# Kernel optimization log

Hardware: AMD Instinct MI355X
Metric: run time of the kernel (lower is better)

The kernel has to match this reference:

```python
import jax, jax.numpy as jnp
import numpy as np
from math import sqrt

E = 1024          # embedding_size
A = 64            # attention_size (per-head)
H = E // A        # 16 heads
FF = 4 * E        # 4096
B, S = 2, 2048
EPS = 1e-5


def layernorm(x, g, b):
    mu = jnp.mean(x, axis=-1, keepdims=True)
    var = jnp.mean(jnp.square(x - mu), axis=-1, keepdims=True)
    return (x - mu) * jax.lax.rsqrt(var + EPS) * g + b


def setup_inputs() -> dict:
    key = jax.random.key(0)
    ks = jax.random.split(key, 12)
    s = 0.02
    return {
        "embedding": jax.random.normal(ks[0], (B, S, E), jnp.float32),
        "positional_encoding": jax.random.normal(ks[1], (B, S, E), jnp.float32),
        # per-head QKV projections (no bias), stacked over heads: [H, E, A]
        "Wq": jax.random.normal(ks[2], (H, E, A), jnp.float32) * s,
        "Wk": jax.random.normal(ks[3], (H, E, A), jnp.float32) * s,
        "Wv": jax.random.normal(ks[4], (H, E, A), jnp.float32) * s,
        "Wproj": jax.random.normal(ks[5], (E, E), jnp.float32) * s,  # no bias
        "W1": jax.random.normal(ks[6], (E, FF), jnp.float32) * s,
        "b1": jnp.zeros((FF,), jnp.float32),
        "W2": jax.random.normal(ks[7], (FF, E), jnp.float32) * s,
        "b2": jnp.zeros((E,), jnp.float32),
        # LayerNorm params: attn norm, FFN-internal norm, final FF norm
        "g_attn": jnp.ones((E,), jnp.float32), "be_attn": jnp.zeros((E,), jnp.float32),
        "g_ffn": jnp.ones((E,), jnp.float32), "be_ffn": jnp.zeros((E,), jnp.float32),
        "g_out": jnp.ones((E,), jnp.float32), "be_out": jnp.zeros((E,), jnp.float32),
    }


def reference(embedding, positional_encoding, Wq, Wk, Wv, Wproj, W1, b1, W2, b2,
              g_attn, be_attn, g_ffn, be_ffn, g_out, be_out):
    x = embedding + positional_encoding                       # [B,S,E]
    # All heads at once (original loops over heads; same math):
    Q = jnp.einsum('bse,hea->hbsa', x, Wq)                    # [H,B,S,A]
    K = jnp.einsum('bse,hea->hbsa', x, Wk)
    V = jnp.einsum('bse,hea->hbsa', x, Wv)
    # NOTE: original scales by sqrt(input dim) = sqrt(E), not sqrt(A)
    scale = sqrt(E)
    scores = jnp.einsum('hbsa,hbta->hbst', Q, K) / scale      # [H,B,S,S]
    causal = jnp.tril(jnp.ones((S, S), bool))                 # j >= k allowed
    scores = jnp.where(causal, scores, -jnp.inf)
    probs = jax.nn.softmax(scores, axis=-1)
    attn = jnp.einsum('hbst,hbta->hbsa', probs, V)            # [H,B,S,A]
    # concat heads along feature dim -> [B,S,H*A] = [B,S,E]
    attn = jnp.transpose(attn, (1, 2, 0, 3)).reshape(x.shape[0], x.shape[1], E)
    attn = attn @ Wproj                                       # linear proj, no bias
    mha = layernorm(x + attn, g_attn, be_attn)
    # FeedForward: relu applied AFTER the second linear (as in source)
    hidden = mha @ W1 + b1
    ff = jax.nn.relu(hidden @ W2 + b2)
    ff_out = layernorm(mha + ff, g_ffn, be_ffn)
    encoded = layernorm(mha + ff_out, g_out, be_out)
    return encoded, K, V
```

## Files before the change

### kernel.cpp

```cpp
#include <hip/hip_runtime.h>


typedef unsigned short u16;
typedef unsigned int u32;
typedef __bf16 bf16x8 __attribute__((ext_vector_type(8)));
typedef float f32x4 __attribute__((ext_vector_type(4)));

#define AS1 __attribute__((address_space(1)))
#define AS3 __attribute__((address_space(3)))

__device__ __forceinline__ u16 f2bf(float f) {
    return __builtin_bit_cast(u16, static_cast<__bf16>(f));
}

__device__ __forceinline__ int swz(int row) { return ((row ^ (row >> 2)) & 7) << 4; }

__device__ __forceinline__ void gload16(void* lds, const void* g) {
    __builtin_amdgcn_global_load_lds((const AS1 void*)(unsigned long long)g,
                                     (AS3 void*)(u32)(unsigned long long)lds, 16, 0, 0);
}

template <int BM, int AMODE, int OMODE>
__launch_bounds__(256, (BM == 128) ? 2 : 3)
__global__ void k_mm(const void* Ap, const u16* __restrict__ Bt, int K, int KZ,
                     float* C, float* Cp, const float* __restrict__ bias,
                     const float* resid, const float* resid2,
                     u16* oQb, float* oKf, u16* oKb, float* oVf, int relu) {
    constexpr int MF = BM / 32;
    __shared__ __align__(16) u16 As[2][BM * 64];
    __shared__ __align__(16) u16 Bs[2][128 * 64];
    const int tid = threadIdx.x;
    const int wave = tid >> 6, lane = tid & 63, quad = lane >> 4, l16 = lane & 15;
    const int wm = wave & 1, wn = wave >> 1;
    const int m0 = blockIdx.x * BM, n0 = blockIdx.y * 128;
    const int kbeg = blockIdx.z * KZ;
    const int nk = KZ / 64;

    f32x4 acc[MF][4];
#pragma unroll
    for (int mf = 0; mf < MF; ++mf)
#pragma unroll
        for (int nf = 0; nf < 4; ++nf) acc[mf][nf] = (f32x4){0.f, 0.f, 0.f, 0.f};

    auto stageA = [&](int b, int kk) {
        if constexpr (AMODE == 1) {
            const float* Af = (const float*)Ap;
#pragma unroll
            for (int i = 0; i < BM / 16; ++i) {
                const int slot = tid + i * 256;
                const int row = slot >> 4, c4 = (slot & 15) * 4;
                float4 v = *(const float4*)(Af + (long long)(m0 + row) * K + kk + c4);
                ushort4 s;
                s.x = f2bf(v.x); s.y = f2bf(v.y); s.z = f2bf(v.z); s.w = f2bf(v.w);
                *(ushort4*)((char*)As[b] + row * 128 + ((c4 * 2) ^ swz(row))) = s;
            }
        } else {
            const u16* Ab = (const u16*)Ap;
#pragma unroll
            for (int i = 0; i < BM / 32; ++i) {
                const int chunk = wave * (BM / 32) + i;
                const int row = chunk * 8 + (lane >> 3);
                const int cb = (lane & 7) * 16;
                const int e = kk + ((cb ^ swz(row)) >> 1);
                const u16* src;
                if constexpr (AMODE == 2)
                    src = Ab + (long long)(e >> 6) * 262144 + (long long)(m0 + row) * 64 + (e & 63);
                else
                    src = Ab + (long long)(m0 + row) * K + e;
                gload16((char*)As[b] + chunk * 1024, src);
            }
        }
    };
    auto stageB = [&](int b, int kk) {
#pragma unroll
        for (int i = 0; i < 4; ++i) {
            const int chunk = wave * 4 + i;
            const int row = chunk * 8 + (lane >> 3);
            const int cb = (lane & 7) * 16;
            gload16((char*)Bs[b] + chunk * 1024,
                    Bt + (long long)(n0 + row) * K + kk + ((cb ^ swz(row)) >> 1));
        }
    };

    stageA(0, kbeg);
    stageB(0, kbeg);
    int cur = 0;
    for (int t = 0; t < nk; ++t) {
        __syncthreads();
        if (t + 1 < nk) {
            stageA(cur ^ 1, kbeg + (t + 1) * 64);
            stageB(cur ^ 1, kbeg + (t + 1) * 64);
        }
#pragma unroll
        for (int ks = 0; ks < 2; ++ks) {
            bf16x8 af[MF], bfr[4];
#pragma unroll
            for (int mf = 0; mf < MF; ++mf) {
                const int row = wm * (BM / 2) + mf * 16 + l16;
                af[mf] = *(const bf16x8*)((const char*)As[cur] + row * 128 +
                                          ((ks * 64 + quad * 16) ^ swz(row)));
            }
#pragma unroll
            for (int nf = 0; nf < 4; ++nf) {
                const int row = wn * 64 + nf * 16 + l16;
                bfr[nf] = *(const bf16x8*)((const char*)Bs[cur] + row * 128 +
                                           ((ks * 64 + quad * 16) ^ swz(row)));
            }
#pragma unroll
            for (int mf = 0; mf < MF; ++mf)
#pragma unroll
                for (int nf = 0; nf < 4; ++nf)
                    acc[mf][nf] = __builtin_amdgcn_mfma_f32_16x16x32_bf16(af[mf], bfr[nf],
                                                                          acc[mf][nf], 0, 0, 0);
        }
        cur ^= 1;
    }

#pragma unroll
    for (int mf = 0; mf < MF; ++mf) {
#pragma unroll
        for (int nf = 0; nf < 4; ++nf) {
#pragma unroll
            for (int r = 0; r < 4; ++r) {
                const long long row = m0 + wm * (BM / 2) + mf * 16 + quad * 4 + r;
                const int col = n0 + wn * 64 + nf * 16 + l16;
                float v = acc[mf][nf][r];
                if constexpr (OMODE == 0) {
                    if (bias) v += bias[col];
                    if (relu) v = fmaxf(v, 0.f);
                    if (resid) v += resid[row * 1024 + col];
                    if (resid2) v += resid2[row * 1024 + col];
                    C[row * 1024 + col] = v;
                } else if constexpr (OMODE == 1) {
                    const int sel = col >> 10, h = (col >> 6) & 15, a = col & 63;
                    const long long idx = (long long)h * 262144 + row * 64 + a;
                    if (sel == 0) oQb[idx] = f2bf(v);
                    else if (sel == 1) { oKf[idx] = v; oKb[idx] = f2bf(v); }
                    else oVf[idx] = v;
                } else {
                    Cp[(long long)blockIdx.z * 1048576 + (long long)col * 1024 + row] = v;
                }
            }
        }
    }
}

__global__ void k_prep(const float* __restrict__ emb, const float* __restrict__ pos,
                       const float* __restrict__ W1, const float* __restrict__ W2,
                       const float* __restrict__ Wq, const float* __restrict__ Wk,
                       const float* __restrict__ Wv, const float* __restrict__ Wp,
                       const float* __restrict__ b2,
                       u16* __restrict__ xb, u16* __restrict__ W1b,
                       u16* __restrict__ W2t, u16* __restrict__ WBt,
                       u16* __restrict__ WpT, float* __restrict__ b12) {
    __shared__ float T[64][65];
    const int bx = blockIdx.x, tid = threadIdx.x;
    if (bx < 8192) {
        const long long i = ((long long)(bx & 4095) * 256 + tid) * 4;
        const float* a = (bx < 4096) ? emb : W1;
        u16* o = (bx < 4096) ? xb : W1b;
        float4 v = *(const float4*)(a + i);
        if (bx < 4096) {
            float4 u = *(const float4*)(pos + i);
            v.x += u.x; v.y += u.y; v.z += u.z; v.w += u.w;
        }
        ushort4 s;
        s.x = f2bf(v.x); s.y = f2bf(v.y); s.z = f2bf(v.z); s.w = f2bf(v.w);
        *(ushort4*)(o + i) = s;
        return;
    }
    if (bx == 10240) {
        float4 v = *(const float4*)(b2 + tid * 4);
        *(float4*)(b12 + tid * 4) = v;
        return;
    }
    const float* ip;
    u16* op;
    long long ldin, ldout;
    if (bx < 9216) {
        const int t = bx - 8192, x = t & 63, z = t >> 6;
        ip = W2 + (long long)z * 64 + (long long)x * 65536;
        ldin = 1024;
        op = W2t + (long long)z * 262144 + x * 64;
        ldout = 4096;
    } else {
        const int t = bx - 9216, x = t & 15, z = t >> 4;
        const int w = z >> 4, h = z & 15;
        if (w < 3) {
            ip = (w == 0 ? Wq : (w == 1 ? Wk : Wv)) + h * 65536 + x * 4096;
            ldin = 64;
            op = WBt + (long long)(w * 16 + h) * 65536 + x * 64;
        } else {
            ip = Wp + x * 65536 + h * 64;
            ldin = 1024;
            op = WpT + (long long)h * 65536 + x * 64;
        }
        ldout = 1024;
    }
#pragma unroll
    for (int i = 0; i < 4; ++i) {
        const int slot = tid + i * 256;
        const int r = slot >> 4, c4 = (slot & 15) * 4;
        float4 v = *(const float4*)(ip + (long long)r * ldin + c4);
        T[r][c4] = v.x; T[r][c4 + 1] = v.y; T[r][c4 + 2] = v.z; T[r][c4 + 3] = v.w;
    }
    __syncthreads();
#pragma unroll
    for (int i = 0; i < 4; ++i) {
        const int slot = tid + i * 256;
        const int c = slot >> 4, r4 = (slot & 15) * 4;
        ushort4 s;
        s.x = f2bf(T[r4][c]); s.y = f2bf(T[r4 + 1][c]);
        s.z = f2bf(T[r4 + 2][c]); s.w = f2bf(T[r4 + 3][c]);
        *(ushort4*)(op + (long long)c * ldout + r4) = s;
    }
}

__global__ void k_tc(const float* __restrict__ in, u16* __restrict__ out,
                     long long ldin, long long ldout, long long szin, long long szout) {
    __shared__ float T[64][65];
    const int x = blockIdx.x, z = blockIdx.y, tid = threadIdx.x;
    const float* ip = in + (long long)z * szin + (long long)x * 64 * ldin;
    u16* op = out + (long long)z * szout + (long long)x * 64;
#pragma unroll
    for (int i = 0; i < 4; ++i) {
        const int slot = tid + i * 256;
        const int r = slot >> 4, c4 = (slot & 15) * 4;
        float4 v = *(const float4*)(ip + (long long)r * ldin + c4);
        T[r][c4] = v.x; T[r][c4 + 1] = v.y; T[r][c4 + 2] = v.z; T[r][c4 + 3] = v.w;
    }
    __syncthreads();
#pragma unroll
    for (int i = 0; i < 4; ++i) {
        const int slot = tid + i * 256;
        const int c = slot >> 4, r4 = (slot & 15) * 4;
        ushort4 s;
        s.x = f2bf(T[r4][c]); s.y = f2bf(T[r4 + 1][c]);
        s.z = f2bf(T[r4 + 2][c]); s.w = f2bf(T[r4 + 3][c]);
        *(ushort4*)(op + (long long)c * ldout + r4) = s;
    }
}

__global__ void k_rb(const float* __restrict__ P, u16* __restrict__ out,
                     const float* __restrict__ b1, const float* __restrict__ W2,
                     float* __restrict__ b12) {
    const int bx = blockIdx.x, tid = threadIdx.x;
    if (bx < 1024) {
        const long long i = ((long long)bx * 256 + tid) * 4;
        float4 a = *(const float4*)(P + i);
        float4 b = *(const float4*)(P + i + 1048576);
        float4 c = *(const float4*)(P + i + 2097152);
        float4 d = *(const float4*)(P + i + 3145728);
        ushort4 s;
        s.x = f2bf(a.x + b.x + c.x + d.x); s.y = f2bf(a.y + b.y + c.y + d.y);
        s.z = f2bf(a.z + b.z + c.z + d.z); s.w = f2bf(a.w + b.w + c.w + d.w);
        *(ushort4*)(out + i) = s;
    } else {
        const int z = bx - 1024;
        const int o4 = tid * 4;
        const float* Wr = W2 + (long long)z * 16384 + o4;
        float ax = 0.f, ay = 0.f, az = 0.f, aw = 0.f;
#pragma unroll
        for (int ff = 0; ff < 16; ++ff) {
            const float bb = b1[z * 16 + ff];
            float4 w = *(const float4*)(Wr + ff * 1024);
            ax += bb * w.x; ay += bb * w.y; az += bb * w.z; aw += bb * w.w;
        }
        atomicAdd(b12 + o4, ax);
        atomicAdd(b12 + o4 + 1, ay);
        atomicAdd(b12 + o4 + 2, az);
        atomicAdd(b12 + o4 + 3, aw);
    }
}

__launch_bounds__(512, 2)
__global__ void k_flash(u16* Qb, const u16* __restrict__ Kb, const u16* __restrict__ Vg) {
    __shared__ __align__(16) u16 Ks[2][64 * 64];
    __shared__ __align__(16) u16 Vs[2][64 * 64];
    __shared__ __align__(16) u16 Pb[8][16 * 64];
    const int tid = threadIdx.x;
    const int wave = tid >> 6, lane = tid & 63, quad = lane >> 4, l16 = lane & 15;
    const int hb = blockIdx.y, h = hb >> 1, b = hb & 1;
    const int xr = 15 - (int)blockIdx.x;
    const int q0 = xr * 128;
    const long long qbase = (long long)h * 262144 + (long long)b * 131072;
    u16* Qp = Qb + qbase + (long long)q0 * 64;
    const u16* Kp = Kb + qbase;
    const u16* Vp = Vg + (long long)hb * 131072;
    const float NEG = -1.0e30f;

    const int qrow = wave * 16 + l16;
    const bf16x8 aq0 = *(const bf16x8*)(Qp + qrow * 64 + quad * 8);
    const bf16x8 aq1 = *(const bf16x8*)(Qp + qrow * 64 + 32 + quad * 8);

    f32x4 o[4];
#pragma unroll
    for (int g = 0; g < 4; ++g) o[g] = (f32x4){0.f, 0.f, 0.f, 0.f};
    float mrun = NEG, lrun = 0.f;
    u16* Pw = Pb[wave];

    auto stage = [&](int bi, int k0) {
        const int row = tid >> 3;
        const int cb = (tid & 7) * 16;
        const int eo = (cb ^ swz(row)) >> 1;
        gload16((char*)Ks[bi] + tid * 16, Kp + (long long)(k0 + row) * 64 + eo);
        gload16((char*)Vs[bi] + tid * 16, Vp + (long long)row * 2048 + k0 + eo);
    };

    const int nit = 2 * xr + 2;
    stage(0, 0);
    int cur = 0;
    for (int it = 0; it < nit; ++it) {
        __syncthreads();
        if (it + 1 < nit) stage(cur ^ 1, (it + 1) * 64);
        f32x4 sc[4];
        __builtin_amdgcn_s_setprio(1);
#pragma unroll
        for (int kg = 0; kg < 4; ++kg) {
            const int krow = kg * 16 + l16;
            const bf16x8 bka = *(const bf16x8*)((const char*)Ks[cur] + krow * 128 +
                                                ((quad * 16) ^ swz(krow)));
            const bf16x8 bkb = *(const bf16x8*)((const char*)Ks[cur] + krow * 128 +
                                                ((64 + quad * 16) ^ swz(krow)));
            sc[kg] = (f32x4){0.f, 0.f, 0.f, 0.f};
            sc[kg] = __builtin_amdgcn_mfma_f32_16x16x32_bf16(bka, aq0, sc[kg], 0, 0, 0);
            sc[kg] = __builtin_amdgcn_mfma_f32_16x16x32_bf16(bkb, aq1, sc[kg], 0, 0, 0);
        }
        __builtin_amdgcn_s_setprio(0);
        const int k0 = it * 64;
        const int q = q0 + wave * 16 + l16;
        const bool edge = (it >= nit - 2);
        float vv[4][4];
        float tmax = NEG;
#pragma unroll
        for (int kg = 0; kg < 4; ++kg)
#pragma unroll
            for (int r = 0; r < 4; ++r) {
                float x = sc[kg][r] * 0.03125f;
                if (edge && (k0 + kg * 16 + quad * 4 + r > q)) x = NEG;
                vv[kg][r] = x;
                tmax = fmaxf(tmax, x);
            }
        tmax = fmaxf(tmax, __shfl_xor(tmax, 16));
        tmax = fmaxf(tmax, __shfl_xor(tmax, 32));
        if (__all(tmax - mrun <= 8.f)) {
            float rs = 0.f;
#pragma unroll
            for (int kg = 0; kg < 4; ++kg)
#pragma unroll
                for (int r = 0; r < 4; ++r) {
                    const float e = __expf(vv[kg][r] - mrun);
                    vv[kg][r] = e;
                    rs += e;
                }
            rs += __shfl_xor(rs, 16);
            rs += __shfl_xor(rs, 32);
            lrun += rs;
        } else {
            const float mn = fmaxf(mrun, tmax);
            const float alpha = __expf(mrun - mn);
            mrun = mn;
            float rs = 0.f;
#pragma unroll
            for (int kg = 0; kg < 4; ++kg)
#pragma unroll
                for (int r = 0; r < 4; ++r) {
                    const float e = __expf(vv[kg][r] - mn);
                    vv[kg][r] = e;
                    rs += e;
                }
            rs += __shfl_xor(rs, 16);
            rs += __shfl_xor(rs, 32);
            lrun = lrun * alpha + rs;
#pragma unroll
            for (int r = 0; r < 4; ++r) {
                const float ar = __shfl(alpha, quad * 4 + r, 16);
#pragma unroll
                for (int g = 0; g < 4; ++g) o[g][r] *= ar;
            }
        }
#pragma unroll
        for (int kg = 0; kg < 4; ++kg) {
            ushort4 s;
            s.x = f2bf(vv[kg][0]); s.y = f2bf(vv[kg][1]);
            s.z = f2bf(vv[kg][2]); s.w = f2bf(vv[kg][3]);
            *(ushort4*)((char*)Pw + l16 * 128 + ((kg * 32 + quad * 8) ^ swz(l16))) = s;
        }
        const bf16x8 ap0 = *(const bf16x8*)((const char*)Pw + l16 * 128 +
                                            ((quad * 16) ^ swz(l16)));
        const bf16x8 ap1 = *(const bf16x8*)((const char*)Pw + l16 * 128 +
                                            ((64 + quad * 16) ^ swz(l16)));
        __builtin_amdgcn_s_setprio(1);
#pragma unroll
        for (int g = 0; g < 4; ++g) {
            const int ar = g * 16 + l16;
            const bf16x8 bv0 = *(const bf16x8*)((const char*)Vs[cur] + ar * 128 +
                                                ((quad * 16) ^ swz(ar)));
            const bf16x8 bv1 = *(const bf16x8*)((const char*)Vs[cur] + ar * 128 +
                                                ((64 + quad * 16) ^ swz(ar)));
            o[g] = __builtin_amdgcn_mfma_f32_16x16x32_bf16(ap0, bv0, o[g], 0, 0, 0);
            o[g] = __builtin_amdgcn_mfma_f32_16x16x32_bf16(ap1, bv1, o[g], 0, 0, 0);
        }
        __builtin_amdgcn_s_setprio(0);
        cur ^= 1;
    }

#pragma unroll
    for (int r = 0; r < 4; ++r) {
        const float lr = __shfl(lrun, quad * 4 + r, 16);
        const float inv = 1.0f / lr;
        const int srow = wave * 16 + quad * 4 + r;
#pragma unroll
        for (int g = 0; g < 4; ++g)
            Qp[srow * 64 + g * 16 + l16] = f2bf(o[g][r] * inv);
    }
}

__global__ void k_ln(const float* in1, const float* in2,
                     const float* __restrict__ g, const float* __restrict__ be,
                     float* out) {
    __shared__ float red[8];
    const int m = blockIdx.x, tid = threadIdx.x, e0 = tid * 4;
    const long long bp = (long long)m * 1024;
    float4 v = *(const float4*)(in1 + bp + e0);
    if (in2) {
        float4 u = *(const float4*)(in2 + bp + e0);
        v.x += u.x; v.y += u.y; v.z += u.z; v.w += u.w;
    }
    float s1 = v.x + v.y + v.z + v.w;
    float s2 = v.x * v.x + v.y * v.y + v.z * v.z + v.w * v.w;
#pragma unroll
    for (int off = 1; off < 64; off <<= 1) { s1 += __shfl_xor(s1, off); s2 += __shfl_xor(s2, off); }
    if ((tid & 63) == 0) { red[tid >> 6] = s1; red[4 + (tid >> 6)] = s2; }
    __syncthreads();
    const float S1 = red[0] + red[1] + red[2] + red[3];
    const float S2 = red[4] + red[5] + red[6] + red[7];
    const float mean = S1 * (1.0f / 1024.0f);
    const float var = S2 * (1.0f / 1024.0f) - mean * mean;
    const float rstd = rsqrtf(var + 1e-5f);
    float4 ug = *(const float4*)(g + e0);
    float4 ub = *(const float4*)(be + e0);
    float4 o;
    o.x = (v.x - mean) * rstd * ug.x + ub.x;
    o.y = (v.y - mean) * rstd * ug.y + ub.y;
    o.z = (v.z - mean) * rstd * ug.z + ub.z;
    o.w = (v.w - mean) * rstd * ug.w + ub.w;
    *(float4*)(out + bp + e0) = o;
}

__global__ void k_ln23(const float* r2, const float* __restrict__ mha,
                       const float* __restrict__ g1, const float* __restrict__ be1,
                       const float* __restrict__ g2, const float* __restrict__ be2,
                       float* out) {
    __shared__ float red[8];
    const int m = blockIdx.x, tid = threadIdx.x, e0 = tid * 4;
    const long long bp = (long long)m * 1024;
    float4 v = *(const float4*)(r2 + bp + e0);
    float s1 = v.x + v.y + v.z + v.w;
    float s2 = v.x * v.x + v.y * v.y + v.z * v.z + v.w * v.w;
#pragma unroll
    for (int off = 1; off < 64; off <<= 1) { s1 += __shfl_xor(s1, off); s2 += __shfl_xor(s2, off); }
    if ((tid & 63) == 0) { red[tid >> 6] = s1; red[4 + (tid >> 6)] = s2; }
    __syncthreads();
    float S1 = red[0] + red[1] + red[2] + red[3];
    float S2 = red[4] + red[5] + red[6] + red[7];
    float mean = S1 * (1.0f / 1024.0f);
    float rstd = rsqrtf(S2 * (1.0f / 1024.0f) - mean * mean + 1e-5f);
    float4 ug = *(const float4*)(g1 + e0);
    float4 ub = *(const float4*)(be1 + e0);
    float4 vm = *(const float4*)(mha + bp + e0);
    float4 t;
    t.x = vm.x + (v.x - mean) * rstd * ug.x + ub.x;
    t.y = vm.y + (v.y - mean) * rstd * ug.y + ub.y;
    t.z = vm.z + (v.z - mean) * rstd * ug.z + ub.z;
    t.w = vm.w + (v.w - mean) * rstd * ug.w + ub.w;
    s1 = t.x + t.y + t.z + t.w;
    s2 = t.x * t.x + t.y * t.y + t.z * t.z + t.w * t.w;
#pragma unroll
    for (int off = 1; off < 64; off <<= 1) { s1 += __shfl_xor(s1, off); s2 += __shfl_xor(s2, off); }
    __syncthreads();
    if ((tid & 63) == 0) { red[tid >> 6] = s1; red[4 + (tid >> 6)] = s2; }
    __syncthreads();
    S1 = red[0] + red[1] + red[2] + red[3];
    S2 = red[4] + red[5] + red[6] + red[7];
    mean = S1 * (1.0f / 1024.0f);
    rstd = rsqrtf(S2 * (1.0f / 1024.0f) - mean * mean + 1e-5f);
    ug = *(const float4*)(g2 + e0);
    ub = *(const float4*)(be2 + e0);
    float4 oo;
    oo.x = (t.x - mean) * rstd * ug.x + ub.x;
    oo.y = (t.y - mean) * rstd * ug.y + ub.y;
    oo.z = (t.z - mean) * rstd * ug.z + ub.z;
    oo.w = (t.w - mean) * rstd * ug.w + ub.w;
    *(float4*)(out + bp + e0) = oo;
}

extern "C" void kernel_launch(void* const* d_in, const int* in_sizes, int n_in,
                              void* d_out, int out_size, void* d_ws, size_t ws_size,
                              hipStream_t stream) {
    (void)in_sizes; (void)n_in; (void)out_size; (void)ws_size;
    const float* emb    = (const float*)d_in[0];
    const float* pos    = (const float*)d_in[1];
    const float* Wq     = (const float*)d_in[2];
    const float* Wk     = (const float*)d_in[3];
    const float* Wv     = (const float*)d_in[4];
    const float* Wproj  = (const float*)d_in[5];
    const float* W1     = (const float*)d_in[6];
    const float* b1     = (const float*)d_in[7];
    const float* W2     = (const float*)d_in[8];
    const float* b2     = (const float*)d_in[9];
    const float* g_attn = (const float*)d_in[10];
    const float* be_attn= (const float*)d_in[11];
    const float* g_ffn  = (const float*)d_in[12];
    const float* be_ffn = (const float*)d_in[13];
    const float* g_out  = (const float*)d_in[14];
    const float* be_out = (const float*)d_in[15];

    float* enc   = (float*)d_out;
    float* out_K = enc + 4194304;
    float* out_V = enc + 8388608;
    u16* QbU  = (u16*)enc;
    u16* KbU  = (u16*)enc + 4194304;
    u16* W1b  = (u16*)enc;
    u16* W2t  = (u16*)enc + 4194304;
    float* Ppart = out_K;

    u16* wsu    = (u16*)d_ws;
    u16* WBt    = wsu;
    u16* xb     = wsu + 4194304;
    u16* VbT    = wsu;
    u16* WpT    = wsu + 8388608;
    u16* W12T   = wsu + 9437184;
    float* b12  = (float*)(wsu + 10485760);
    float* res1 = (float*)d_ws;

    k_prep<<<10241, 256, 0, stream>>>(emb, pos, W1, W2, Wq, Wk, Wv, Wproj, b2,
                                      xb, W1b, W2t, WBt, WpT, b12);
    k_mm<64, 0, 2><<<dim3(16, 8, 4), 256, 0, stream>>>(W1b, W2t, 4096, 1024,
        nullptr, Ppart, nullptr, nullptr, nullptr, nullptr, nullptr, nullptr, nullptr, 0);
    k_rb<<<1280, 256, 0, stream>>>(Ppart, W12T, b1, W2, b12);

    k_mm<128, 0, 1><<<dim3(32, 24), 256, 0, stream>>>(xb, WBt, 1024, 1024,
        nullptr, nullptr, nullptr, nullptr, nullptr, QbU, out_K, KbU, out_V, 0);
    k_tc<<<dim3(32, 32), 256, 0, stream>>>(out_V, VbT, 64, 2048, 131072, 131072);

    k_flash<<<dim3(16, 32), 512, 0, stream>>>(QbU, KbU, VbT);

    k_mm<64, 2, 0><<<dim3(64, 8), 256, 0, stream>>>(QbU, WpT, 1024, 1024,
        res1, nullptr, nullptr, emb, pos, nullptr, nullptr, nullptr, nullptr, 0);
    k_ln<<<4096, 256, 0, stream>>>(res1, nullptr, g_attn, be_attn, res1);

    k_mm<64, 1, 0><<<dim3(64, 8), 256, 0, stream>>>(res1, W12T, 1024, 1024,
        enc, nullptr, b12, res1, nullptr, nullptr, nullptr, nullptr, nullptr, 1);
    k_ln23<<<4096, 256, 0, stream>>>(enc, res1, g_ffn, be_ffn, g_out, be_out, enc);
}
```

Baseline: 364.7 us.

## Triple-buffer GEMM loads, fold softmax scale into Q, use exp2

For all GEMMs except the fp32-input one, the double-buffered k-loop becomes a three-stage LDS pipeline. It waits with an explicit vmcnt and a raw barrier, so two tiles of global-to-LDS loads stay in flight while the current tile is computed. The QKV projection moves to 64-row tiles, doubling its block count. The attention softmax scale and log2(e) are folded into Q when it is written as bf16, so the flash loop drops its per-element multiply and uses hardware exp2. The causal-mask branch is split out of the unmasked fast path. The costs are more LDS per block (which may lower occupancy), a hand-counted vmcnt that only holds for BM=64, and slightly different rounding of Q.

Result: slower. 374.8 us (+2.8%).

```diff
diff --git a/kernel.cpp b/kernel.cpp
--- a/kernel.cpp
+++ b/kernel.cpp
@@ -13,6 +13,8 @@
     return __builtin_bit_cast(u16, static_cast<__bf16>(f));
 }
 
+__device__ __forceinline__ float exp2hw(float x) { return __builtin_amdgcn_exp2f(x); }
+
 __device__ __forceinline__ int swz(int row) { return ((row ^ (row >> 2)) & 7) << 4; }
 
 __device__ __forceinline__ void gload16(void* lds, const void* g) {
@@ -20,15 +22,18 @@
                                      (AS3 void*)(u32)(unsigned long long)lds, 16, 0, 0);
 }
 
+#define QSCALE 0.0450842200886f
+
 template <int BM, int AMODE, int OMODE>
-__launch_bounds__(256, (BM == 128) ? 2 : 3)
+__launch_bounds__(256, (AMODE == 1) ? 3 : 2)
 __global__ void k_mm(const void* Ap, const u16* __restrict__ Bt, int K, int KZ,
                      float* C, float* Cp, const float* __restrict__ bias,
                      const float* resid, const float* resid2,
                      u16* oQb, float* oKf, u16* oKb, float* oVf, int relu) {
     constexpr int MF = BM / 32;
-    __shared__ __align__(16) u16 As[2][BM * 64];
-    __shared__ __align__(16) u16 Bs[2][128 * 64];
+    constexpr int NBUF = (AMODE == 1) ? 2 : 3;
+    __shared__ __align__(16) u16 As[NBUF][BM * 64];
+    __shared__ __align__(16) u16 Bs[NBUF][128 * 64];
     const int tid = threadIdx.x;
     const int wave = tid >> 6, lane = tid & 63, quad = lane >> 4, l16 = lane & 15;
     const int wm = wave & 1, wn = wave >> 1;
@@ -81,29 +86,20 @@
                     Bt + (long long)(n0 + row) * K + kk + ((cb ^ swz(row)) >> 1));
         }
     };
-
-    stageA(0, kbeg);
-    stageB(0, kbeg);
-    int cur = 0;
-    for (int t = 0; t < nk; ++t) {
-        __syncthreads();
-        if (t + 1 < nk) {
-            stageA(cur ^ 1, kbeg + (t + 1) * 64);
-            stageB(cur ^ 1, kbeg + (t + 1) * 64);
-        }
+    auto compute = [&](int b) {
 #pragma unroll
         for (int ks = 0; ks < 2; ++ks) {
             bf16x8 af[MF], bfr[4];
 #pragma unroll
             for (int mf = 0; mf < MF; ++mf) {
                 const int row = wm * (BM / 2) + mf * 16 + l16;
-                af[mf] = *(const bf16x8*)((const char*)As[cur] + row * 128 +
+                af[mf] = *(const bf16x8*)((const char*)As[b] + row * 128 +
                                           ((ks * 64 + quad * 16) ^ swz(row)));
             }
 #pragma unroll
             for (int nf = 0; nf < 4; ++nf) {
                 const int row = wn * 64 + nf * 16 + l16;
-                bfr[nf] = *(const bf16x8*)((const char*)Bs[cur] + row * 128 +
+                bfr[nf] = *(const bf16x8*)((const char*)Bs[b] + row * 128 +
                                            ((ks * 64 + quad * 16) ^ swz(row)));
             }
 #pragma unroll
@@ -113,7 +109,43 @@
                     acc[mf][nf] = __builtin_amdgcn_mfma_f32_16x16x32_bf16(af[mf], bfr[nf],
                                                                           acc[mf][nf], 0, 0, 0);
         }
-        cur ^= 1;
+    };
+
+    if constexpr (AMODE == 1) {
+        stageA(0, kbeg);
+        stageB(0, kbeg);
+        int cur = 0;
+        for (int t = 0; t < nk; ++t) {
+            __syncthreads();
+            if (t + 1 < nk) {
+                stageA(cur ^ 1, kbeg + (t + 1) * 64);
+                stageB(cur ^ 1, kbeg + (t + 1) * 64);
+            }
+            compute(cur);
+            cur ^= 1;
+        }
+    } else {
+        stageA(0, kbeg);
+        stageB(0, kbeg);
+        if (nk > 1) { stageA(1, kbeg + 64); stageB(1, kbeg + 64); }
+        int cur = 0;
+        for (int t = 0; t < nk; ++t) {
+            if (t < nk - 1) {
+                asm volatile("s_waitcnt vmcnt(6)" ::: "memory");
+            } else {
+                asm volatile("s_waitcnt vmcnt(0)" ::: "memory");
+            }
+            __builtin_amdgcn_s_barrier();
+            __builtin_amdgcn_sched_barrier(0);
+            if (t + 2 < nk) {
+                const int nxt = (cur >= 1) ? cur - 1 : cur + 2;
+                stageA(nxt, kbeg + (t + 2) * 64);
+                stageB(nxt, kbeg + (t + 2) * 64);
+            }
+            __builtin_amdgcn_sched_barrier(0);
+            compute(cur);
+            cur = (cur == 2) ? 0 : cur + 1;
+        }
     }
 
 #pragma unroll
@@ -134,7 +166,7 @@
                 } else if constexpr (OMODE == 1) {
                     const int sel = col >> 10, h = (col >> 6) & 15, a = col & 63;
                     const long long idx = (long long)h * 262144 + row * 64 + a;
-                    if (sel == 0) oQb[idx] = f2bf(v);
+                    if (sel == 0) oQb[idx] = f2bf(v * QSCALE);
                     else if (sel == 1) { oKf[idx] = v; oKb[idx] = f2bf(v); }
                     else oVf[idx] = v;
                 } else {
@@ -329,18 +361,27 @@
         __builtin_amdgcn_s_setprio(0);
         const int k0 = it * 64;
         const int q = q0 + wave * 16 + l16;
-        const bool edge = (it >= nit - 2);
         float vv[4][4];
         float tmax = NEG;
-#pragma unroll
-        for (int kg = 0; kg < 4; ++kg)
-#pragma unroll
-            for (int r = 0; r < 4; ++r) {
-                float x = sc[kg][r] * 0.03125f;
-                if (edge && (k0 + kg * 16 + quad * 4 + r > q)) x = NEG;
-                vv[kg][r] = x;
-                tmax = fmaxf(tmax, x);
-            }
+        if (it >= nit - 2) {
+#pragma unroll
+            for (int kg = 0; kg < 4; ++kg)
+#pragma unroll
+                for (int r = 0; r < 4; ++r) {
+                    float x = sc[kg][r];
+                    if (k0 + kg * 16 + quad * 4 + r > q) x = NEG;
+                    vv[kg][r] = x;
+                    tmax = fmaxf(tmax, x);
+                }
+        } else {
+#pragma unroll
+            for (int kg = 0; kg < 4; ++kg)
+#pragma unroll
+                for (int r = 0; r < 4; ++r) {
+                    vv[kg][r] = sc[kg][r];
+                    tmax = fmaxf(tmax, sc[kg][r]);
+                }
+        }
         tmax = fmaxf(tmax, __shfl_xor(tmax, 16));
         tmax = fmaxf(tmax, __shfl_xor(tmax, 32));
         if (__all(tmax - mrun <= 8.f)) {
@@ -349,7 +390,7 @@
             for (int kg = 0; kg < 4; ++kg)
 #pragma unroll
                 for (int r = 0; r < 4; ++r) {
-                    const float e = __expf(vv[kg][r] - mrun);
+                    const float e = exp2hw(vv[kg][r] - mrun);
                     vv[kg][r] = e;
                     rs += e;
                 }
@@ -358,14 +399,14 @@
             lrun += rs;
         } else {
             const float mn = fmaxf(mrun, tmax);
-            const float alpha = __expf(mrun - mn);
+            const float alpha = exp2hw(mrun - mn);
             mrun = mn;
             float rs = 0.f;
 #pragma unroll
             for (int kg = 0; kg < 4; ++kg)
 #pragma unroll
                 for (int r = 0; r < 4; ++r) {
-                    const float e = __expf(vv[kg][r] - mn);
+                    const float e = exp2hw(vv[kg][r] - mn);
                     vv[kg][r] = e;
                     rs += e;
                 }
@@ -540,7 +581,7 @@
         nullptr, Ppart, nullptr, nullptr, nullptr, nullptr, nullptr, nullptr, nullptr, 0);
     k_rb<<<1280, 256, 0, stream>>>(Ppart, W12T, b1, W2, b12);
 
-    k_mm<128, 0, 1><<<dim3(32, 24), 256, 0, stream>>>(xb, WBt, 1024, 1024,
+    k_mm<64, 0, 1><<<dim3(64, 24), 256, 0, stream>>>(xb, WBt, 1024, 1024,
         nullptr, nullptr, nullptr, nullptr, nullptr, QbU, out_K, KbU, out_V, 0);
     k_tc<<<dim3(32, 32), 256, 0, stream>>>(out_V, VbT, 64, 2048, 131072, 131072);
 
```

## Pair causal flash query tiles per block and fold softmax scale into Q

Applied to the files above, without the earlier changes.

The flash attention grid is halved, and each block now processes two query tiles (15-x and x). This gives every block the same total causal work and cuts the tail imbalance. The 1/32 softmax scale times log2(e) is folded into Q when it is stored in the QKV GEMM epilogue, so the inner loop can use a raw hardware exp2 with no per-element multiply. The mask branch is also split so non-edge iterations skip the mask test. Risks are fewer blocks in flight (256) and slight precision changes from scaling Q before the bf16 rounding.

New measurement: 356.6 us. 2.2% less time.

```diff
diff --git a/kernel.cpp b/kernel.cpp
--- a/kernel.cpp
+++ b/kernel.cpp
@@ -13,12 +13,16 @@
     return __builtin_bit_cast(u16, static_cast<__bf16>(f));
 }
 
+__device__ __forceinline__ float exp2hw(float x) { return __builtin_amdgcn_exp2f(x); }
+
 __device__ __forceinline__ int swz(int row) { return ((row ^ (row >> 2)) & 7) << 4; }
 
 __device__ __forceinline__ void gload16(void* lds, const void* g) {
     __builtin_amdgcn_global_load_lds((const AS1 void*)(unsigned long long)g,
                                      (AS3 void*)(u32)(unsigned long long)lds, 16, 0, 0);
 }
+
+#define QSCALE 0.0450842200886f
 
 template <int BM, int AMODE, int OMODE>
 __launch_bounds__(256, (BM == 128) ? 2 : 3)
@@ -81,6 +85,30 @@
                     Bt + (long long)(n0 + row) * K + kk + ((cb ^ swz(row)) >> 1));
         }
     };
+    auto compute = [&](int b) {
+#pragma unroll
+        for (int ks = 0; ks < 2; ++ks) {
+            bf16x8 af[MF], bfr[4];
+#pragma unroll
+            for (int mf = 0; mf < MF; ++mf) {
+                const int row = wm * (BM / 2) + mf * 16 + l16;
+                af[mf] = *(const bf16x8*)((const char*)As[b] + row * 128 +
+                                          ((ks * 64 + quad * 16) ^ swz(row)));
+            }
+#pragma unroll
+            for (int nf = 0; nf < 4; ++nf) {
+                const int row = wn * 64 + nf * 16 + l16;
+                bfr[nf] = *(const bf16x8*)((const char*)Bs[b] + row * 128 +
+                                           ((ks * 64 + quad * 16) ^ swz(row)));
+            }
+#pragma unroll
+            for (int mf = 0; mf < MF; ++mf)
+#pragma unroll
+                for (int nf = 0; nf < 4; ++nf)
+                    acc[mf][nf] = __builtin_amdgcn_mfma_f32_16x16x32_bf16(af[mf], bfr[nf],
+                                                                          acc[mf][nf], 0, 0, 0);
+        }
+    };
 
     stageA(0, kbeg);
     stageB(0, kbeg);
@@ -91,28 +119,7 @@
             stageA(cur ^ 1, kbeg + (t + 1) * 64);
             stageB(cur ^ 1, kbeg + (t + 1) * 64);
         }
-#pragma unroll
-        for (int ks = 0; ks < 2; ++ks) {
-            bf16x8 af[MF], bfr[4];
-#pragma unroll
-            for (int mf = 0; mf < MF; ++mf) {
-                const int row = wm * (BM / 2) + mf * 16 + l16;
-                af[mf] = *(const bf16x8*)((const char*)As[cur] + row * 128 +
-                                          ((ks * 64 + quad * 16) ^ swz(row)));
-            }
-#pragma unroll
-            for (int nf = 0; nf < 4; ++nf) {
-                const int row = wn * 64 + nf * 16 + l16;
-                bfr[nf] = *(const bf16x8*)((const char*)Bs[cur] + row * 128 +
-                                           ((ks * 64 + quad * 16) ^ swz(row)));
-            }
-#pragma unroll
-            for (int mf = 0; mf < MF; ++mf)
-#pragma unroll
-                for (int nf = 0; nf < 4; ++nf)
-                    acc[mf][nf] = __builtin_amdgcn_mfma_f32_16x16x32_bf16(af[mf], bfr[nf],
-                                                                          acc[mf][nf], 0, 0, 0);
-        }
+        compute(cur);
         cur ^= 1;
     }
 
@@ -134,7 +141,7 @@
                 } else if constexpr (OMODE == 1) {
                     const int sel = col >> 10, h = (col >> 6) & 15, a = col & 63;
                     const long long idx = (long long)h * 262144 + row * 64 + a;
-                    if (sel == 0) oQb[idx] = f2bf(v);
+                    if (sel == 0) oQb[idx] = f2bf(v * QSCALE);
                     else if (sel == 1) { oKf[idx] = v; oKb[idx] = f2bf(v); }
                     else oVf[idx] = v;
                 } else {
@@ -281,139 +288,153 @@
     const int tid = threadIdx.x;
     const int wave = tid >> 6, lane = tid & 63, quad = lane >> 4, l16 = lane & 15;
     const int hb = blockIdx.y, h = hb >> 1, b = hb & 1;
-    const int xr = 15 - (int)blockIdx.x;
-    const int q0 = xr * 128;
     const long long qbase = (long long)h * 262144 + (long long)b * 131072;
-    u16* Qp = Qb + qbase + (long long)q0 * 64;
     const u16* Kp = Kb + qbase;
     const u16* Vp = Vg + (long long)hb * 131072;
     const float NEG = -1.0e30f;
-
-    const int qrow = wave * 16 + l16;
-    const bf16x8 aq0 = *(const bf16x8*)(Qp + qrow * 64 + quad * 8);
-    const bf16x8 aq1 = *(const bf16x8*)(Qp + qrow * 64 + 32 + quad * 8);
-
-    f32x4 o[4];
-#pragma unroll
-    for (int g = 0; g < 4; ++g) o[g] = (f32x4){0.f, 0.f, 0.f, 0.f};
-    float mrun = NEG, lrun = 0.f;
     u16* Pw = Pb[wave];
 
-    auto stage = [&](int bi, int k0) {
-        const int row = tid >> 3;
-        const int cb = (tid & 7) * 16;
-        const int eo = (cb ^ swz(row)) >> 1;
-        gload16((char*)Ks[bi] + tid * 16, Kp + (long long)(k0 + row) * 64 + eo);
-        gload16((char*)Vs[bi] + tid * 16, Vp + (long long)row * 2048 + k0 + eo);
+    auto run_phase = [&](int xr) {
+        const int q0 = xr * 128;
+        u16* Qp = Qb + qbase + (long long)q0 * 64;
+        const int qrow = wave * 16 + l16;
+        const bf16x8 aq0 = *(const bf16x8*)(Qp + qrow * 64 + quad * 8);
+        const bf16x8 aq1 = *(const bf16x8*)(Qp + qrow * 64 + 32 + quad * 8);
+
+        f32x4 o[4];
+#pragma unroll
+        for (int g = 0; g < 4; ++g) o[g] = (f32x4){0.f, 0.f, 0.f, 0.f};
+        float mrun = NEG, lrun = 0.f;
+
+        auto stage = [&](int bi, int k0) {
+            const int row = tid >> 3;
+            const int cb = (tid & 7) * 16;
+            const int eo = (cb ^ swz(row)) >> 1;
+            gload16((char*)Ks[bi] + tid * 16, Kp + (long long)(k0 + row) * 64 + eo);
+            gload16((char*)Vs[bi] + tid * 16, Vp + (long long)row * 2048 + k0 + eo);
+        };
+
+        const int nit = 2 * xr + 2;
+        __syncthreads();
+        stage(0, 0);
+        int cur = 0;
+        for (int it = 0; it < nit; ++it) {
+            __syncthreads();
+            if (it + 1 < nit) stage(cur ^ 1, (it + 1) * 64);
+            f32x4 sc[4];
+            __builtin_amdgcn_s_setprio(1);
+#pragma unroll
+            for (int kg = 0; kg < 4; ++kg) {
+                const int krow = kg * 16 + l16;
+                const bf16x8 bka = *(const bf16x8*)((const char*)Ks[cur] + krow * 128 +
+                                                    ((quad * 16) ^ swz(krow)));
+                const bf16x8 bkb = *(const bf16x8*)((const char*)Ks[cur] + krow * 128 +
+                                                    ((64 + quad * 16) ^ swz(krow)));
+                sc[kg] = (f32x4){0.f, 0.f, 0.f, 0.f};
+                sc[kg] = __builtin_amdgcn_mfma_f32_16x16x32_bf16(bka, aq0, sc[kg], 0, 0, 0);
+                sc[kg] = __builtin_amdgcn_mfma_f32_16x16x32_bf16(bkb, aq1, sc[kg], 0, 0, 0);
+            }
+            __builtin_amdgcn_s_setprio(0);
+            const int k0 = it * 64;
+            const int q = q0 + wave * 16 + l16;
+            float vv[4][4];
+            float tmax = NEG;
+            if (it >= nit - 2) {
+#pragma unroll
+                for (int kg = 0; kg < 4; ++kg)
+#pragma unroll
+                    for (int r = 0; r < 4; ++r) {
+                        float x = sc[kg][r];
+                        if (k0 + kg * 16 + quad * 4 + r > q) x = NEG;
+                        vv[kg][r] = x;
+                        tmax = fmaxf(tmax, x);
+                    }
+            } else {
+#pragma unroll
+                for (int kg = 0; kg < 4; ++kg)
+#pragma unroll
+                    for (int r = 0; r < 4; ++r) {
+                        vv[kg][r] = sc[kg][r];
+                        tmax = fmaxf(tmax, sc[kg][r]);
+                    }
+            }
+            tmax = fmaxf(tmax, __shfl_xor(tmax, 16));
+            tmax = fmaxf(tmax, __shfl_xor(tmax, 32));
+            if (__all(tmax - mrun <= 8.f)) {
+                float rs = 0.f;
+#pragma unroll
+                for (int kg = 0; kg < 4; ++kg)
+#pragma unroll
+                    for (int r = 0; r < 4; ++r) {
+                        const float e = exp2hw(vv[kg][r] - mrun);
+                        vv[kg][r] = e;
+                        rs += e;
+                    }
+                rs += __shfl_xor(rs, 16);
+                rs += __shfl_xor(rs, 32);
+                lrun += rs;
+            } else {
+                const float mn = fmaxf(mrun, tmax);
+                const float alpha = exp2hw(mrun - mn);
+                mrun = mn;
+                float rs = 0.f;
+#pragma unroll
+                for (int kg = 0; kg < 4; ++kg)
+#pragma unroll
+                    for (int r = 0; r < 4; ++r) {
+                        const float e = exp2hw(vv[kg][r] - mn);
+                        vv[kg][r] = e;
+                        rs += e;
+                    }
+                rs += __shfl_xor(rs, 16);
+                rs += __shfl_xor(rs, 32);
+                lrun = lrun * alpha + rs;
+#pragma unroll
+                for (int r = 0; r < 4; ++r) {
+                    const float ar = __shfl(alpha, quad * 4 + r, 16);
+#pragma unroll
+                    for (int g = 0; g < 4; ++g) o[g][r] *= ar;
+                }
+            }
+#pragma unroll
+            for (int kg = 0; kg < 4; ++kg) {
+                ushort4 s;
+                s.x = f2bf(vv[kg][0]); s.y = f2bf(vv[kg][1]);
+                s.z = f2bf(vv[kg][2]); s.w = f2bf(vv[kg][3]);
+                *(ushort4*)((char*)Pw + l16 * 128 + ((kg * 32 + quad * 8) ^ swz(l16))) = s;
+            }
+            const bf16x8 ap0 = *(const bf16x8*)((const char*)Pw + l16 * 128 +
+                                                ((quad * 16) ^ swz(l16)));
+            const bf16x8 ap1 = *(const bf16x8*)((const char*)Pw + l16 * 128 +
+                                                ((64 + quad * 16) ^ swz(l16)));
+            __builtin_amdgcn_s_setprio(1);
+#pragma unroll
+            for (int g = 0; g < 4; ++g) {
+                const int ar = g * 16 + l16;
+                const bf16x8 bv0 = *(const bf16x8*)((const char*)Vs[cur] + ar * 128 +
+                                                    ((quad * 16) ^ swz(ar)));
+                const bf16x8 bv1 = *(const bf16x8*)((const char*)Vs[cur] + ar * 128 +
+                                                    ((64 + quad * 16) ^ swz(ar)));
+                o[g] = __builtin_amdgcn_mfma_f32_16x16x32_bf16(ap0, bv0, o[g], 0, 0, 0);
+                o[g] = __builtin_amdgcn_mfma_f32_16x16x32_bf16(ap1, bv1, o[g], 0, 0, 0);
+            }
+            __builtin_amdgcn_s_setprio(0);
+            cur ^= 1;
+        }
+
+#pragma unroll
+        for (int r = 0; r < 4; ++r) {
+            const float lr = __shfl(lrun, quad * 4 + r, 16);
+            const float inv = 1.0f / lr;
+            const int srow = wave * 16 + quad * 4 + r;
+#pragma unroll
+            for (int g = 0; g < 4; ++g)
+                Qp[srow * 64 + g * 16 + l16] = f2bf(o[g][r] * inv);
+        }
     };
 
-    const int nit = 2 * xr + 2;
-    stage(0, 0);
-    int cur = 0;
-    for (int it = 0; it < nit; ++it) {
-        __syncthreads();
-        if (it + 1 < nit) stage(cur ^ 1, (it + 1) * 64);
-        f32x4 sc[4];
-        __builtin_amdgcn_s_setprio(1);
-#pragma unroll
-        for (int kg = 0; kg < 4; ++kg) {
-            const int krow = kg * 16 + l16;
-            const bf16x8 bka = *(const bf16x8*)((const char*)Ks[cur] + krow * 128 +
-                                                ((quad * 16) ^ swz(krow)));
-            const bf16x8 bkb = *(const bf16x8*)((const char*)Ks[cur] + krow * 128 +
-                                                ((64 + quad * 16) ^ swz(krow)));
-            sc[kg] = (f32x4){0.f, 0.f, 0.f, 0.f};
-            sc[kg] = __builtin_amdgcn_mfma_f32_16x16x32_bf16(bka, aq0, sc[kg], 0, 0, 0);
-            sc[kg] = __builtin_amdgcn_mfma_f32_16x16x32_bf16(bkb, aq1, sc[kg], 0, 0, 0);
-        }
-        __builtin_amdgcn_s_setprio(0);
-        const int k0 = it * 64;
-        const int q = q0 + wave * 16 + l16;
-        const bool edge = (it >= nit - 2);
-        float vv[4][4];
-        float tmax = NEG;
-#pragma unroll
-        for (int kg = 0; kg < 4; ++kg)
-#pragma unroll
-            for (int r = 0; r < 4; ++r) {
-                float x = sc[kg][r] * 0.03125f;
-                if (edge && (k0 + kg * 16 + quad * 4 + r > q)) x = NEG;
-                vv[kg][r] = x;
-                tmax = fmaxf(tmax, x);
-            }
-        tmax = fmaxf(tmax, __shfl_xor(tmax, 16));
-        tmax = fmaxf(tmax, __shfl_xor(tmax, 32));
-        if (__all(tmax - mrun <= 8.f)) {
-            float rs = 0.f;
-#pragma unroll
-            for (int kg = 0; kg < 4; ++kg)
-#pragma unroll
-                for (int r = 0; r < 4; ++r) {
-                    const float e = __expf(vv[kg][r] - mrun);
-                    vv[kg][r] = e;
-                    rs += e;
-                }
-            rs += __shfl_xor(rs, 16);
-            rs += __shfl_xor(rs, 32);
-            lrun += rs;
-        } else {
-            const float mn = fmaxf(mrun, tmax);
-            const float alpha = __expf(mrun - mn);
-            mrun = mn;
-            float rs = 0.f;
-#pragma unroll
-            for (int kg = 0; kg < 4; ++kg)
-#pragma unroll
-                for (int r = 0; r < 4; ++r) {
-                    const float e = __expf(vv[kg][r] - mn);
-                    vv[kg][r] = e;
-                    rs += e;
-                }
-            rs += __shfl_xor(rs, 16);
-            rs += __shfl_xor(rs, 32);
-            lrun = lrun * alpha + rs;
-#pragma unroll
-            for (int r = 0; r < 4; ++r) {
-                const float ar = __shfl(alpha, quad * 4 + r, 16);
-#pragma unroll
-                for (int g = 0; g < 4; ++g) o[g][r] *= ar;
-            }
-        }
-#pragma unroll
-        for (int kg = 0; kg < 4; ++kg) {
-            ushort4 s;
-            s.x = f2bf(vv[kg][0]); s.y = f2bf(vv[kg][1]);
-            s.z = f2bf(vv[kg][2]); s.w = f2bf(vv[kg][3]);
-            *(ushort4*)((char*)Pw + l16 * 128 + ((kg * 32 + quad * 8) ^ swz(l16))) = s;
-        }
-        const bf16x8 ap0 = *(const bf16x8*)((const char*)Pw + l16 * 128 +
-                                            ((quad * 16) ^ swz(l16)));
-        const bf16x8 ap1 = *(const bf16x8*)((const char*)Pw + l16 * 128 +
-                                            ((64 + quad * 16) ^ swz(l16)));
-        __builtin_amdgcn_s_setprio(1);
-#pragma unroll
-        for (int g = 0; g < 4; ++g) {
-            const int ar = g * 16 + l16;
-            const bf16x8 bv0 = *(const bf16x8*)((const char*)Vs[cur] + ar * 128 +
-                                                ((quad * 16) ^ swz(ar)));
-            const bf16x8 bv1 = *(const bf16x8*)((const char*)Vs[cur] + ar * 128 +
-                                                ((64 + quad * 16) ^ swz(ar)));
-            o[g] = __builtin_amdgcn_mfma_f32_16x16x32_bf16(ap0, bv0, o[g], 0, 0, 0);
-            o[g] = __builtin_amdgcn_mfma_f32_16x16x32_bf16(ap1, bv1, o[g], 0, 0, 0);
-        }
-        __builtin_amdgcn_s_setprio(0);
-        cur ^= 1;
-    }
-
-#pragma unroll
-    for (int r = 0; r < 4; ++r) {
-        const float lr = __shfl(lrun, quad * 4 + r, 16);
-        const float inv = 1.0f / lr;
-        const int srow = wave * 16 + quad * 4 + r;
-#pragma unroll
-        for (int g = 0; g < 4; ++g)
-            Qp[srow * 64 + g * 16 + l16] = f2bf(o[g][r] * inv);
-    }
+    run_phase(15 - (int)blockIdx.x);
+    run_phase((int)blockIdx.x);
 }
 
 __global__ void k_ln(const float* in1, const float* in2,
@@ -544,7 +565,7 @@
         nullptr, nullptr, nullptr, nullptr, nullptr, QbU, out_K, KbU, out_V, 0);
     k_tc<<<dim3(32, 32), 256, 0, stream>>>(out_V, VbT, 64, 2048, 131072, 131072);
 
-    k_flash<<<dim3(16, 32), 512, 0, stream>>>(QbU, KbU, VbT);
+    k_flash<<<dim3(8, 32), 512, 0, stream>>>(QbU, KbU, VbT);
 
     k_mm<64, 2, 0><<<dim3(64, 8), 256, 0, stream>>>(QbU, WpT, 1024, 1024,
         res1, nullptr, nullptr, emb, pos, nullptr, nullptr, nullptr, nullptr, 0);
```
